# Kernel tuning notes

Measured on AMD Instinct MI355X. Metric: run time of the kernel, lower is better.

The kernel has to match this reference:

```python
import math
import jax, jax.numpy as jnp
import numpy as np

# Model hyperparameters (match init_kwargs)
LAYERS, BLOCKS = 10, 4
RC, DC, SC = 32, 32, 256          # residual / dilation / skip channels
CLASSES, L, K = 256, 1024, 3      # classes, input_length, kernel_size
B = 64                            # batch


def _dilations():
    """Replicates the (new_dilation, init_dilation) schedule built in __init__."""
    ds = []
    init = 1
    for _b in range(BLOCKS):
        d = 1
        for _i in range(LAYERS):
            ds.append((d, init))
            init = d
            d *= 2
    return ds


def dilate(x, dilation, init_dilation):
    """Faithful port of the torch dilate(): (n,c,l) -> (n*d/d0, c, l*d0/d)
    via permute/view/permute, zero-padding the start if l is not divisible."""
    n, c, l = x.shape
    if dilation == init_dilation:
        return x
    factor = dilation / init_dilation
    new_l = int(np.ceil(l / factor) * factor)
    if new_l != l:  # constant_pad_1d with pad_start=True
        x = jnp.pad(x, ((0, 0), (0, 0), (new_l - l, 0)))
        l = new_l
    l_new = int(math.ceil(l * init_dilation / dilation))
    n_new = int(math.ceil(n * dilation / init_dilation))
    x = jnp.transpose(x, (1, 2, 0)).reshape(c, l_new, n_new)  # (c, l, n) contiguous view
    return jnp.transpose(x, (2, 0, 1))


def conv1d(x, w, pad):
    # x: (N, Cin, L), w: (Cout, Cin, K)
    return jax.lax.conv_general_dilated(
        x, w, window_strides=(1,), padding=[(pad, pad)],
        dimension_numbers=("NCH", "OIH", "NCH"))


def setup_inputs() -> dict:
    key = jax.random.key(0)
    ks = jax.random.split(key, 8)
    NL = LAYERS * BLOCKS
    return {
        "input": jax.random.normal(ks[0], (B, 2, L), jnp.float32),
        "start_w": jax.random.normal(ks[1], (RC, 2, 1), jnp.float32) * 0.3,
        "filter_w": jax.random.normal(ks[2], (NL, DC, RC, K), jnp.float32) * 0.1,
        "gate_w": jax.random.normal(ks[3], (NL, DC, RC, K), jnp.float32) * 0.1,
        "res_w": jax.random.normal(ks[4], (NL, RC, DC, 1), jnp.float32) * 0.1,
        "skip_w": jax.random.normal(ks[5], (NL, SC, DC, 1), jnp.float32) * 0.1,
        "fc_w": jax.random.normal(ks[6], (CLASSES, SC * L), jnp.float32) * 0.002,
        "fc_b": jnp.zeros((CLASSES,), jnp.float32),
    }


def reference(input, start_w, filter_w, gate_w, res_w, skip_w, fc_w, fc_b):
    pad = K // 2
    x = conv1d(input, start_w, 0)  # (B, RC, L)
    skip = None
    for i, (d, d0) in enumerate(_dilations()):
        residual = dilate(x, d, d0)                              # fast-wavenet reshape
        f = jnp.tanh(conv1d(residual, filter_w[i], pad))
        g = jax.nn.sigmoid(conv1d(residual, gate_w[i], pad))
        x = f * g                                                # gated activation
        s = x if x.shape[2] == 1 else dilate(x, 1, d)            # undo dilation for skip
        s = conv1d(s, skip_w[i], 0)                              # (B, SC, L)
        skip = s if skip is None else s + skip[:, :, -s.shape[2]:]
        x = conv1d(x, res_w[i], 0) + residual                    # residual connection
    out = jax.nn.relu(skip.reshape(skip.shape[0], -1))           # (B, SC*L)
    return out @ fc_w.T + fc_b                                   # (B, CLASSES)
```

## Files before the change

### kernel.cpp

```cpp
#include <hip/hip_runtime.h>
#include <stdint.h>

typedef short bf16x8 __attribute__((ext_vector_type(8)));
typedef short s4 __attribute__((ext_vector_type(4)));
typedef float f32x4 __attribute__((ext_vector_type(4)));

#define NPOS 65536
#define MB (1024ull * 1024ull)
#define SK_PIECE 2097152

__device__ __forceinline__ unsigned short f32_bf16(float f) {
    union { float f; unsigned u; } v; v.f = f;
    unsigned u = v.u;
    u += 0x7fffu + ((u >> 16) & 1u);
    return (unsigned short)(u >> 16);
}

__device__ __forceinline__ s4 pk4_bf16(float a, float b, float c, float d) {
    union { unsigned u[2]; s4 v; } r;
    asm("v_cvt_pk_bf16_f32 %0, %1, %2" : "=v"(r.u[0]) : "v"(a), "v"(b));
    asm("v_cvt_pk_bf16_f32 %0, %1, %2" : "=v"(r.u[1]) : "v"(c), "v"(d));
    return r.v;
}

__device__ __forceinline__ bf16x8 ldf8_bf16(const float* p) {
    const float4 lo = *(const float4*)p;
    const float4 hi = *(const float4*)(p + 4);
    bf16x8 v;
    v[0] = (short)f32_bf16(lo.x); v[1] = (short)f32_bf16(lo.y);
    v[2] = (short)f32_bf16(lo.z); v[3] = (short)f32_bf16(lo.w);
    v[4] = (short)f32_bf16(hi.x); v[5] = (short)f32_bf16(hi.y);
    v[6] = (short)f32_bf16(hi.z); v[7] = (short)f32_bf16(hi.w);
    return v;
}

__global__ void ws_probe_k(float* __restrict__ out, float mib) {
    int i = blockIdx.x * 256 + threadIdx.x;
    if (i < 16384) out[i] = mib;
}

__global__ void repack_fgw_k(const float* __restrict__ fw,
                             const float* __restrict__ gw,
                             unsigned short* __restrict__ out) {
    int idx = blockIdx.x * 256 + threadIdx.x;
    int ic = idx & 31;
    int r1 = idx >> 5;
    int oc = r1 & 63;
    int r2 = r1 >> 6;
    int k  = r2 % 3;
    int i  = r2 / 3;
    const float* src = (oc < 32) ? fw : gw;
    out[idx] = f32_bf16(src[(((i * 32 + (oc & 31)) * 32 + ic) * 3) + k]);
}

__global__ void repack_sw_k(const float* __restrict__ sw,
                            unsigned short* __restrict__ out) {
    int idx = blockIdx.x * 256 + threadIdx.x;
    out[idx] = f32_bf16(sw[idx]);
}

__global__ void repack_rw_k(const float* __restrict__ rw,
                            unsigned short* __restrict__ out) {
    int idx = blockIdx.x * 256 + threadIdx.x;
    out[idx] = f32_bf16(rw[idx]);
}

__global__ __launch_bounds__(512, 2) void wavenet_rows_k(
    const float* __restrict__ in,
    const float* __restrict__ stw,
    const unsigned short* __restrict__ fgw_all,
    const unsigned short* __restrict__ rwb_all,
    unsigned short* __restrict__ xg_all)
{
    __shared__ __align__(16) unsigned short xb16[1024 * 32];
    __shared__ __align__(16) unsigned short stage[8 * 640];

    const int tid = threadIdx.x;
    const int w = tid >> 6, lane = tid & 63;
    const int quad = lane >> 4, l15 = lane & 15;
    const int b = blockIdx.x;
    const f32x4 zero = {0.f, 0.f, 0.f, 0.f};
    const int c0lo = quad >> 1;
    const int bi   = (quad & 1) * 4;

    float xreg[8][8];

    {
        float s0[8], s1[8];
#pragma unroll
        for (int j = 0; j < 8; ++j) {
            int c = (j < 4) ? (quad * 4 + j) : (16 + quad * 4 + (j - 4));
            s0[j] = stw[c * 2 + 0];
            s1[j] = stw[c * 2 + 1];
        }
#pragma unroll
        for (int g = 0; g < 8; ++g) {
            int t = (w * 8 + g) * 16 + l15;
            float i0 = in[(b * 2 + 0) * 1024 + t];
            float i1 = in[(b * 2 + 1) * 1024 + t];
#pragma unroll
            for (int j = 0; j < 8; ++j) xreg[g][j] = s0[j] * i0 + s1[j] * i1;
            s4 lo = pk4_bf16(xreg[g][0], xreg[g][1], xreg[g][2], xreg[g][3]);
            s4 hi = pk4_bf16(xreg[g][4], xreg[g][5], xreg[g][6], xreg[g][7]);
            int base = t * 32;
            *(s4*)(xb16 + base + ((c0lo ^ (t & 3)) * 8) + bi) = lo;
            *(s4*)(xb16 + base + (((c0lo + 2) ^ (t & 3)) * 8) + bi) = hi;
        }
    }
    __syncthreads();

    unsigned short* const st = stage + w * 640;

#pragma unroll 1
    for (int i = 0; i < 40; ++i) {
        const int d = 1 << (i % 10);
        const unsigned short* fgw = fgw_all + (size_t)i * 6144;
        unsigned short* xg = xg_all + (size_t)i * ((size_t)NPOS * 32)
                                    + (size_t)b * 1024 * 32;
        const bool dores = (i < 39);

        bf16x8 wf[3][2], wg[3][2], wr[2];
#pragma unroll
        for (int k = 0; k < 3; ++k) {
            const unsigned short* wb = fgw + k * 2048;
#pragma unroll
            for (int mt = 0; mt < 2; ++mt) {
                wf[k][mt] = *(const bf16x8*)(wb + (mt * 16 + l15) * 32 + quad * 8);
                wg[k][mt] = *(const bf16x8*)(wb + ((mt + 2) * 16 + l15) * 32 + quad * 8);
            }
        }
        if (dores) {
            const unsigned short* rwb = rwb_all + (size_t)i * 1024;
#pragma unroll
            for (int rt = 0; rt < 2; ++rt)
                wr[rt] = *(const bf16x8*)(rwb + (rt * 16 + l15) * 32 + quad * 8);
        }

#pragma unroll
        for (int g = 0; g < 8; ++g) {
            const int tg = (w * 8 + g) * 16;
            const int tc = tg + l15;

            bf16x8 bfr[3];
            bf16x8 zz; 
#pragma unroll
            for (int j = 0; j < 8; ++j) zz[j] = 0;
            bfr[1] = *(const bf16x8*)(xb16 + tc * 32 + ((quad ^ (tc & 3)) * 8));
            {
                int ts = tc - d, tsc = ts & 1023;
                bf16x8 rv = *(const bf16x8*)(xb16 + tsc * 32 + ((quad ^ (tsc & 3)) * 8));
                bfr[0] = (ts >= 0) ? rv : zz;
            }
            {
                int ts = tc + d, tsc = ts & 1023;
                bf16x8 rv = *(const bf16x8*)(xb16 + tsc * 32 + ((quad ^ (tsc & 3)) * 8));
                bfr[2] = (ts < 1024) ? rv : zz;
            }

            f32x4 accf[2] = {zero, zero};
            f32x4 accg[2] = {zero, zero};
#pragma unroll
            for (int k = 0; k < 3; ++k) {
#pragma unroll
                for (int mt = 0; mt < 2; ++mt) {
                    accf[mt] = __builtin_amdgcn_mfma_f32_16x16x32_bf16(wf[k][mt], bfr[k], accf[mt], 0, 0, 0);
                    accg[mt] = __builtin_amdgcn_mfma_f32_16x16x32_bf16(wg[k][mt], bfr[k], accg[mt], 0, 0, 0);
                }
            }

#pragma unroll
            for (int mt = 0; mt < 2; ++mt) {
                float gv0, gv1, gv2, gv3;
                {
                    float o[4];
#pragma unroll
                    for (int r = 0; r < 4; ++r) {
                        float fv = accf[mt][r], gg = accg[mt][r];
                        float ef = __expf(2.0f * fv);
                        float th = 1.0f - 2.0f * __builtin_amdgcn_rcpf(1.0f + ef);
                        float eg = __expf(-gg);
                        float sg = __builtin_amdgcn_rcpf(1.0f + eg);
                        o[r] = th * sg;
                    }
                    gv0 = o[0]; gv1 = o[1]; gv2 = o[2]; gv3 = o[3];
                }
                *(s4*)(st + l15 * 40 + mt * 16 + quad * 4) = pk4_bf16(gv0, gv1, gv2, gv3);
            }

            if (dores) {
                bf16x8 bx = *(const bf16x8*)(st + l15 * 40 + quad * 8);
                f32x4 accr[2] = {zero, zero};
#pragma unroll
                for (int rt = 0; rt < 2; ++rt)
                    accr[rt] = __builtin_amdgcn_mfma_f32_16x16x32_bf16(wr[rt], bx, accr[rt], 0, 0, 0);
#pragma unroll
                for (int rt = 0; rt < 2; ++rt)
#pragma unroll
                    for (int r = 0; r < 4; ++r)
                        xreg[g][rt * 4 + r] += accr[rt][r];
            }

            {
                int pp = lane >> 2, cc = (lane & 3) * 8;
                int4 v = *(const int4*)(st + pp * 40 + cc);
                *(int4*)(xg + (size_t)(tg + pp) * 32 + cc) = v;
            }
        }
        __syncthreads();

        if (dores) {
#pragma unroll
            for (int g = 0; g < 8; ++g) {
                int t = (w * 8 + g) * 16 + l15;
                s4 lo = pk4_bf16(xreg[g][0], xreg[g][1], xreg[g][2], xreg[g][3]);
                s4 hi = pk4_bf16(xreg[g][4], xreg[g][5], xreg[g][6], xreg[g][7]);
                int base = t * 32;
                *(s4*)(xb16 + base + ((c0lo ^ (t & 3)) * 8) + bi) = lo;
                *(s4*)(xb16 + base + (((c0lo + 2) ^ (t & 3)) * 8) + bi) = hi;
            }
            __syncthreads();
        }
    }
}

__global__ __launch_bounds__(256) void skip_gemm_k(
    const unsigned short* __restrict__ xg_all,
    const unsigned short* __restrict__ swb,
    unsigned short* __restrict__ sk)
{
    __shared__ __align__(16) unsigned short lds[256 * 72];
    int tid = threadIdx.x;
    int w = tid >> 6, lane = tid & 63;
    int quad = lane >> 4, l15 = lane & 15;
    int p0 = blockIdx.x * 64;
    f32x4 zero = {0.f, 0.f, 0.f, 0.f};
    f32x4 acc[4][4];
#pragma unroll
    for (int a = 0; a < 4; ++a)
#pragma unroll
        for (int c = 0; c < 4; ++c) acc[a][c] = zero;

    const unsigned short* bbase = xg_all + ((size_t)(p0 + l15)) * 32 + quad * 8;
    const unsigned short* abase = swb + ((size_t)(w * 64 + l15)) * 32 + quad * 8;

    bf16x8 bcur[4], acur[4], bnxt[4], anxt[4];
#pragma unroll
    for (int ct = 0; ct < 4; ++ct) bcur[ct] = *(const bf16x8*)(bbase + ct * 512);
#pragma unroll
    for (int rt = 0; rt < 4; ++rt) acur[rt] = *(const bf16x8*)(abase + rt * 512);

#pragma unroll 2
    for (int i = 0; i < 40; ++i) {
        if (i < 39) {
            const unsigned short* bn = bbase + (size_t)(i + 1) * NPOS * 32;
            const unsigned short* an = abase + (size_t)(i + 1) * 8192;
#pragma unroll
            for (int ct = 0; ct < 4; ++ct) bnxt[ct] = *(const bf16x8*)(bn + ct * 512);
#pragma unroll
            for (int rt = 0; rt < 4; ++rt) anxt[rt] = *(const bf16x8*)(an + rt * 512);
        }
#pragma unroll
        for (int rt = 0; rt < 4; ++rt)
#pragma unroll
            for (int ct = 0; ct < 4; ++ct)
                acc[rt][ct] = __builtin_amdgcn_mfma_f32_16x16x32_bf16(acur[rt], bcur[ct], acc[rt][ct], 0, 0, 0);
#pragma unroll
        for (int ct = 0; ct < 4; ++ct) bcur[ct] = bnxt[ct];
#pragma unroll
        for (int rt = 0; rt < 4; ++rt) acur[rt] = anxt[rt];
    }

#pragma unroll
    for (int rt = 0; rt < 4; ++rt)
#pragma unroll
        for (int ct = 0; ct < 4; ++ct)
#pragma unroll
            for (int r = 0; r < 4; ++r) {
                float v = acc[rt][ct][r];
                v = v > 0.f ? v : 0.f;
                lds[(w * 64 + rt * 16 + quad * 4 + r) * 72 + ct * 16 + l15] = f32_bf16(v);
            }
    __syncthreads();
    {
        size_t pbbase = (size_t)(p0 >> 6) * 2048;
#pragma unroll
        for (int j = 0; j < 8; ++j) {
            int idx = tid + 256 * j;
            int sc = idx >> 3, tc = idx & 7;
            int4 v = *(const int4*)(lds + sc * 72 + tc * 8);
            unsigned short* dst = sk + (size_t)(sc >> 5) * SK_PIECE + pbbase
                                     + (sc & 31) * 64 + tc * 8;
            *(int4*)dst = v;
        }
    }
}

__global__ __launch_bounds__(256) void fc_part_k(
    const unsigned short* __restrict__ sk,
    const float* __restrict__ fw,
    float* __restrict__ part)
{
    int tid = threadIdx.x;
    int w = tid >> 6, lane = tid & 63;
    int quad = lane >> 4, l15 = lane & 15;
    int kb = blockIdx.x;
    int sc = kb >> 1;
    int tbase = (kb & 1) * 512;
    f32x4 zero = {0.f, 0.f, 0.f, 0.f};
    f32x4 acc[4][4];
#pragma unroll
    for (int a = 0; a < 4; ++a)
#pragma unroll
        for (int c = 0; c < 4; ++c) acc[a][c] = zero;

    const unsigned short* skp = sk + (size_t)(sc >> 5) * SK_PIECE + (sc & 31) * 64;

    for (int it = 0; it < 16; ++it) {
        int t = tbase + it * 32 + quad * 8;
        bf16x8 af[4];
#pragma unroll
        for (int rt = 0; rt < 4; ++rt) {
            int bi = rt * 16 + l15;
            af[rt] = *(const bf16x8*)(skp + (size_t)(bi * 16 + (t >> 6)) * 2048 + (t & 63));
        }
#pragma unroll
        for (int ct = 0; ct < 4; ++ct) {
            bf16x8 bw = ldf8_bf16(fw + (size_t)(w * 64 + ct * 16 + l15) * 262144 + sc * 1024 + t);
#pragma unroll
            for (int rt = 0; rt < 4; ++rt)
                acc[rt][ct] = __builtin_amdgcn_mfma_f32_16x16x32_bf16(af[rt], bw, acc[rt][ct], 0, 0, 0);
        }
    }
#pragma unroll
    for (int rt = 0; rt < 4; ++rt)
#pragma unroll
        for (int ct = 0; ct < 4; ++ct)
#pragma unroll
            for (int r = 0; r < 4; ++r) {
                int bb = rt * 16 + quad * 4 + r;
                int cls = w * 64 + ct * 16 + l15;
                part[((size_t)kb * 64 + bb) * 256 + cls] = acc[rt][ct][r];
            }
}

__global__ void fc_reduce_k(const float* __restrict__ part,
                            const float* __restrict__ fb,
                            float* __restrict__ out) {
    int b = blockIdx.x, cls = threadIdx.x;
    float s = fb[cls];
    for (int kb = 0; kb < 512; ++kb)
        s += part[((size_t)kb * 64 + b) * 256 + cls];
    out[b * 256 + cls] = s;
}

extern "C" void kernel_launch(void* const* d_in, const int* in_sizes, int n_in,
                              void* d_out, int out_size, void* d_ws, size_t ws_size,
                              hipStream_t stream) {
    const float* input    = (const float*)d_in[0];
    const float* start_w  = (const float*)d_in[1];
    const float* filter_w = (const float*)d_in[2];
    const float* gate_w   = (const float*)d_in[3];
    const float* res_w    = (const float*)d_in[4];
    const float* skip_w   = (const float*)d_in[5];
    const float* fc_w     = (const float*)d_in[6];
    const float* fc_b     = (const float*)d_in[7];
    float* out = (float*)d_out;

    const size_t REQUIRED = 192 * MB;
    if (ws_size < REQUIRED) {
        ws_probe_k<<<64, 256, 0, stream>>>(out, (float)(ws_size >> 20));
        return;
    }

    char* ws = (char*)d_ws;
    unsigned short* xg_all = (unsigned short*)(ws);
    unsigned short* sk     = (unsigned short*)(ws);
    float*          part   = (float*)(ws + 32 * MB);
    unsigned short* fgw    = (unsigned short*)(ws + 176 * MB);
    unsigned short* swb    = (unsigned short*)(ws + 176 * MB + 512 * 1024);
    unsigned short* rwb    = (unsigned short*)(ws + 178 * MB);

    repack_fgw_k<<<960, 256, 0, stream>>>(filter_w, gate_w, fgw);
    repack_sw_k<<<1280, 256, 0, stream>>>(skip_w, swb);
    repack_rw_k<<<160, 256, 0, stream>>>(res_w, rwb);

    wavenet_rows_k<<<64, 512, 0, stream>>>(input, start_w, fgw, rwb, xg_all);

    skip_gemm_k<<<1024, 256, 0, stream>>>(xg_all, swb, sk);
    fc_part_k<<<512, 256, 0, stream>>>(sk, fc_w, part);
    fc_reduce_k<<<64, 256, 0, stream>>>(part, fc_b, out);
}
```

Baseline: 795.4 us.

## Double-buffer wavenet LDS, widen to 1024 threads, stage FC weights via LDS

The recurrent wavenet kernel now runs 1024 threads per batch row and ping-pongs between two LDS buffers, which removes one barrier per layer. It also permutes the filter, gate and residual weight rows so the gated output can feed the residual MFMA directly from registers, dropping the LDS staging tile. The FC partial kernel prefetches fc weights into a double-buffered LDS tile, converting to bf16 once per block instead of in every wave. The final reduction is split into two kernels for more parallelism, and the tanh and sigmoid are fused into one reciprocal with clamping.

```diff
diff --git a/kernel.cpp b/kernel.cpp
--- a/kernel.cpp
+++ b/kernel.cpp
@@ -23,15 +23,13 @@
     return r.v;
 }
 
-__device__ __forceinline__ bf16x8 ldf8_bf16(const float* p) {
-    const float4 lo = *(const float4*)p;
-    const float4 hi = *(const float4*)(p + 4);
-    bf16x8 v;
-    v[0] = (short)f32_bf16(lo.x); v[1] = (short)f32_bf16(lo.y);
-    v[2] = (short)f32_bf16(lo.z); v[3] = (short)f32_bf16(lo.w);
-    v[4] = (short)f32_bf16(hi.x); v[5] = (short)f32_bf16(hi.y);
-    v[6] = (short)f32_bf16(hi.z); v[7] = (short)f32_bf16(hi.w);
-    return v;
+__device__ __forceinline__ bf16x8 pk8_bf16(const float* v) {
+    union { unsigned u[4]; bf16x8 x; } r;
+    asm("v_cvt_pk_bf16_f32 %0, %1, %2" : "=v"(r.u[0]) : "v"(v[0]), "v"(v[1]));
+    asm("v_cvt_pk_bf16_f32 %0, %1, %2" : "=v"(r.u[1]) : "v"(v[2]), "v"(v[3]));
+    asm("v_cvt_pk_bf16_f32 %0, %1, %2" : "=v"(r.u[2]) : "v"(v[4]), "v"(v[5]));
+    asm("v_cvt_pk_bf16_f32 %0, %1, %2" : "=v"(r.u[3]) : "v"(v[6]), "v"(v[7]));
+    return r.x;
 }
 
 __global__ void ws_probe_k(float* __restrict__ out, float mib) {
@@ -45,12 +43,15 @@
     int idx = blockIdx.x * 256 + threadIdx.x;
     int ic = idx & 31;
     int r1 = idx >> 5;
-    int oc = r1 & 63;
+    int rq = r1 & 63;
     int r2 = r1 >> 6;
     int k  = r2 % 3;
     int i  = r2 / 3;
-    const float* src = (oc < 32) ? fw : gw;
-    out[idx] = f32_bf16(src[(((i * 32 + (oc & 31)) * 32 + ic) * 3) + k]);
+    int part = rq >> 4;
+    int m = rq & 15;
+    int oc = ((m >> 2) << 3) + ((part & 1) << 2) + (m & 3);
+    const float* src = (part < 2) ? fw : gw;
+    out[idx] = f32_bf16(src[(((i * 32 + oc) * 32 + ic) * 3) + k]);
 }
 
 __global__ void repack_sw_k(const float* __restrict__ sw,
@@ -62,64 +63,64 @@
 __global__ void repack_rw_k(const float* __restrict__ rw,
                             unsigned short* __restrict__ out) {
     int idx = blockIdx.x * 256 + threadIdx.x;
-    out[idx] = f32_bf16(rw[idx]);
-}
-
-__global__ __launch_bounds__(512, 2) void wavenet_rows_k(
+    int ic = idx & 31;
+    int r1 = idx >> 5;
+    int rq = r1 & 31;
+    int i  = r1 >> 5;
+    int rt = rq >> 4, m = rq & 15;
+    int oc = ((m >> 2) << 3) + (rt << 2) + (m & 3);
+    out[idx] = f32_bf16(rw[(i * 32 + oc) * 32 + ic]);
+}
+
+#define MFMA16(A, B, C) __builtin_amdgcn_mfma_f32_16x16x32_bf16(A, B, C, 0, 0, 0)
+
+__global__ __launch_bounds__(1024, 4) void wavenet_rows_k(
     const float* __restrict__ in,
     const float* __restrict__ stw,
     const unsigned short* __restrict__ fgw_all,
     const unsigned short* __restrict__ rwb_all,
     unsigned short* __restrict__ xg_all)
 {
-    __shared__ __align__(16) unsigned short xb16[1024 * 32];
-    __shared__ __align__(16) unsigned short stage[8 * 640];
-
+    __shared__ __align__(16) unsigned short xb16[2][1024 * 32];
     const int tid = threadIdx.x;
     const int w = tid >> 6, lane = tid & 63;
     const int quad = lane >> 4, l15 = lane & 15;
     const int b = blockIdx.x;
     const f32x4 zero = {0.f, 0.f, 0.f, 0.f};
-    const int c0lo = quad >> 1;
-    const int bi   = (quad & 1) * 4;
-
-    float xreg[8][8];
+
+    float xreg[4][8];
 
     {
         float s0[8], s1[8];
 #pragma unroll
         for (int j = 0; j < 8; ++j) {
-            int c = (j < 4) ? (quad * 4 + j) : (16 + quad * 4 + (j - 4));
+            int c = quad * 8 + j;
             s0[j] = stw[c * 2 + 0];
             s1[j] = stw[c * 2 + 1];
         }
 #pragma unroll
-        for (int g = 0; g < 8; ++g) {
-            int t = (w * 8 + g) * 16 + l15;
-            float i0 = in[(b * 2 + 0) * 1024 + t];
-            float i1 = in[(b * 2 + 1) * 1024 + t];
+        for (int g = 0; g < 4; ++g) {
+            int t = (w * 4 + g) * 16 + l15;
+            float i0 = in[b * 2048 + t];
+            float i1 = in[b * 2048 + 1024 + t];
 #pragma unroll
             for (int j = 0; j < 8; ++j) xreg[g][j] = s0[j] * i0 + s1[j] * i1;
-            s4 lo = pk4_bf16(xreg[g][0], xreg[g][1], xreg[g][2], xreg[g][3]);
-            s4 hi = pk4_bf16(xreg[g][4], xreg[g][5], xreg[g][6], xreg[g][7]);
-            int base = t * 32;
-            *(s4*)(xb16 + base + ((c0lo ^ (t & 3)) * 8) + bi) = lo;
-            *(s4*)(xb16 + base + (((c0lo + 2) ^ (t & 3)) * 8) + bi) = hi;
+            *(bf16x8*)(xb16[0] + t * 32 + ((quad ^ (t & 3)) * 8)) = pk8_bf16(xreg[g]);
         }
     }
     __syncthreads();
-
-    unsigned short* const st = stage + w * 640;
 
 #pragma unroll 1
     for (int i = 0; i < 40; ++i) {
         const int d = 1 << (i % 10);
         const unsigned short* fgw = fgw_all + (size_t)i * 6144;
         unsigned short* xg = xg_all + (size_t)i * ((size_t)NPOS * 32)
-                                    + (size_t)b * 1024 * 32;
+                                    + (size_t)b * (1024 * 32);
+        const unsigned short* xcur = xb16[i & 1];
+        unsigned short* xnxt = xb16[(i & 1) ^ 1];
         const bool dores = (i < 39);
 
-        bf16x8 wf[3][2], wg[3][2], wr[2];
+        bf16x8 wf[3][2], wg[3][2];
 #pragma unroll
         for (int k = 0; k < 3; ++k) {
             const unsigned short* wb = fgw + k * 2048;
@@ -129,97 +130,89 @@
                 wg[k][mt] = *(const bf16x8*)(wb + ((mt + 2) * 16 + l15) * 32 + quad * 8);
             }
         }
+        bf16x8 wr0, wr1;
         if (dores) {
             const unsigned short* rwb = rwb_all + (size_t)i * 1024;
-#pragma unroll
-            for (int rt = 0; rt < 2; ++rt)
-                wr[rt] = *(const bf16x8*)(rwb + (rt * 16 + l15) * 32 + quad * 8);
-        }
-
-#pragma unroll
-        for (int g = 0; g < 8; ++g) {
-            const int tg = (w * 8 + g) * 16;
+            wr0 = *(const bf16x8*)(rwb + l15 * 32 + quad * 8);
+            wr1 = *(const bf16x8*)(rwb + (16 + l15) * 32 + quad * 8);
+        }
+
+#pragma unroll
+        for (int g = 0; g < 4; ++g) {
+            const int tg = (w * 4 + g) * 16;
             const int tc = tg + l15;
 
-            bf16x8 bfr[3];
-            bf16x8 zz; 
+            bf16x8 zz;
 #pragma unroll
             for (int j = 0; j < 8; ++j) zz[j] = 0;
-            bfr[1] = *(const bf16x8*)(xb16 + tc * 32 + ((quad ^ (tc & 3)) * 8));
-            {
-                int ts = tc - d, tsc = ts & 1023;
-                bf16x8 rv = *(const bf16x8*)(xb16 + tsc * 32 + ((quad ^ (tsc & 3)) * 8));
-                bfr[0] = (ts >= 0) ? rv : zz;
-            }
-            {
-                int ts = tc + d, tsc = ts & 1023;
-                bf16x8 rv = *(const bf16x8*)(xb16 + tsc * 32 + ((quad ^ (tsc & 3)) * 8));
-                bfr[2] = (ts < 1024) ? rv : zz;
-            }
 
             f32x4 accf[2] = {zero, zero};
             f32x4 accg[2] = {zero, zero};
-#pragma unroll
-            for (int k = 0; k < 3; ++k) {
+            {
+                int ts = tc - d, tm = ts & 1023;
+                bf16x8 rv = *(const bf16x8*)(xcur + tm * 32 + ((quad ^ (tm & 3)) * 8));
+                bf16x8 b0 = (ts >= 0) ? rv : zz;
 #pragma unroll
                 for (int mt = 0; mt < 2; ++mt) {
-                    accf[mt] = __builtin_amdgcn_mfma_f32_16x16x32_bf16(wf[k][mt], bfr[k], accf[mt], 0, 0, 0);
-                    accg[mt] = __builtin_amdgcn_mfma_f32_16x16x32_bf16(wg[k][mt], bfr[k], accg[mt], 0, 0, 0);
+                    accf[mt] = MFMA16(wf[0][mt], b0, accf[mt]);
+                    accg[mt] = MFMA16(wg[0][mt], b0, accg[mt]);
                 }
             }
-
-#pragma unroll
-            for (int mt = 0; mt < 2; ++mt) {
-                float gv0, gv1, gv2, gv3;
-                {
-                    float o[4];
-#pragma unroll
-                    for (int r = 0; r < 4; ++r) {
-                        float fv = accf[mt][r], gg = accg[mt][r];
-                        float ef = __expf(2.0f * fv);
-                        float th = 1.0f - 2.0f * __builtin_amdgcn_rcpf(1.0f + ef);
-                        float eg = __expf(-gg);
-                        float sg = __builtin_amdgcn_rcpf(1.0f + eg);
-                        o[r] = th * sg;
-                    }
-                    gv0 = o[0]; gv1 = o[1]; gv2 = o[2]; gv3 = o[3];
+            {
+                bf16x8 b1 = *(const bf16x8*)(xcur + tc * 32 + ((quad ^ (tc & 3)) * 8));
+#pragma unroll
+                for (int mt = 0; mt < 2; ++mt) {
+                    accf[mt] = MFMA16(wf[1][mt], b1, accf[mt]);
+                    accg[mt] = MFMA16(wg[1][mt], b1, accg[mt]);
                 }
-                *(s4*)(st + l15 * 40 + mt * 16 + quad * 4) = pk4_bf16(gv0, gv1, gv2, gv3);
-            }
+            }
+            {
+                int ts = tc + d, tm = ts & 1023;
+                bf16x8 rv = *(const bf16x8*)(xcur + tm * 32 + ((quad ^ (tm & 3)) * 8));
+                bf16x8 b2 = (ts < 1024) ? rv : zz;
+#pragma unroll
+                for (int mt = 0; mt < 2; ++mt) {
+                    accf[mt] = MFMA16(wf[2][mt], b2, accf[mt]);
+                    accg[mt] = MFMA16(wg[2][mt], b2, accg[mt]);
+                }
+            }
+
+            float gv[8];
+#pragma unroll
+            for (int mt = 0; mt < 2; ++mt)
+#pragma unroll
+                for (int r = 0; r < 4; ++r) {
+                    float fv = accf[mt][r], gg = accg[mt][r];
+                    fv = fminf(fmaxf(fv, -10.f), 10.f);
+                    gg = fminf(fmaxf(gg, -15.f), 15.f);
+                    float a = __expf(2.f * fv);
+                    float c = __expf(-gg);
+                    float rr = __builtin_amdgcn_rcpf((a + 1.f) * (1.f + c));
+                    gv[mt * 4 + r] = (a - 1.f) * rr;
+                }
+            bf16x8 bx = pk8_bf16(gv);
+
+            *(bf16x8*)(xg + (size_t)tc * 32 + quad * 8) = bx;
 
             if (dores) {
-                bf16x8 bx = *(const bf16x8*)(st + l15 * 40 + quad * 8);
-                f32x4 accr[2] = {zero, zero};
-#pragma unroll
-                for (int rt = 0; rt < 2; ++rt)
-                    accr[rt] = __builtin_amdgcn_mfma_f32_16x16x32_bf16(wr[rt], bx, accr[rt], 0, 0, 0);
-#pragma unroll
-                for (int rt = 0; rt < 2; ++rt)
-#pragma unroll
-                    for (int r = 0; r < 4; ++r)
-                        xreg[g][rt * 4 + r] += accr[rt][r];
-            }
-
-            {
-                int pp = lane >> 2, cc = (lane & 3) * 8;
-                int4 v = *(const int4*)(st + pp * 40 + cc);
-                *(int4*)(xg + (size_t)(tg + pp) * 32 + cc) = v;
+                f32x4 a0 = MFMA16(wr0, bx, zero);
+                f32x4 a1 = MFMA16(wr1, bx, zero);
+#pragma unroll
+                for (int r = 0; r < 4; ++r) {
+                    xreg[g][r]     += a0[r];
+                    xreg[g][4 + r] += a1[r];
+                }
+            }
+        }
+
+        if (dores) {
+#pragma unroll
+            for (int g = 0; g < 4; ++g) {
+                int t = (w * 4 + g) * 16 + l15;
+                *(bf16x8*)(xnxt + t * 32 + ((quad ^ (t & 3)) * 8)) = pk8_bf16(xreg[g]);
             }
         }
         __syncthreads();
-
-        if (dores) {
-#pragma unroll
-            for (int g = 0; g < 8; ++g) {
-                int t = (w * 8 + g) * 16 + l15;
-                s4 lo = pk4_bf16(xreg[g][0], xreg[g][1], xreg[g][2], xreg[g][3]);
-                s4 hi = pk4_bf16(xreg[g][4], xreg[g][5], xreg[g][6], xreg[g][7]);
-                int base = t * 32;
-                *(s4*)(xb16 + base + ((c0lo ^ (t & 3)) * 8) + bi) = lo;
-                *(s4*)(xb16 + base + (((c0lo + 2) ^ (t & 3)) * 8) + bi) = hi;
-            }
-            __syncthreads();
-        }
     }
 }
 
@@ -300,6 +293,7 @@
     const float* __restrict__ fw,
     float* __restrict__ part)
 {
+    __shared__ __align__(16) unsigned short blds[2][256 * 32];
     int tid = threadIdx.x;
     int w = tid >> 6, lane = tid & 63;
     int quad = lane >> 4, l15 = lane & 15;
@@ -314,8 +308,28 @@
         for (int c = 0; c < 4; ++c) acc[a][c] = zero;
 
     const unsigned short* skp = sk + (size_t)(sc >> 5) * SK_PIECE + (sc & 31) * 64;
-
+    const int cls_s = tid >> 3, kc_s = tid & 7;
+    const float* fwbase = fw + (size_t)cls_s * 262144 + sc * 1024 + tbase + kc_s * 4;
+
+    auto stage = [&](int it, int buf) {
+        float4 v[8];
+#pragma unroll
+        for (int jj = 0; jj < 8; ++jj)
+            v[jj] = *(const float4*)(fwbase + (size_t)jj * 32 * 262144 + it * 32);
+#pragma unroll
+        for (int jj = 0; jj < 8; ++jj) {
+            int cls = cls_s + jj * 32;
+            int slot = (kc_s >> 1) ^ (cls & 3);
+            *(s4*)(blds[buf] + cls * 32 + slot * 8 + (kc_s & 1) * 4) =
+                pk4_bf16(v[jj].x, v[jj].y, v[jj].z, v[jj].w);
+        }
+    };
+
+    stage(0, 0);
+    __syncthreads();
     for (int it = 0; it < 16; ++it) {
+        int buf = it & 1;
+        if (it < 15) stage(it + 1, buf ^ 1);
         int t = tbase + it * 32 + quad * 8;
         bf16x8 af[4];
 #pragma unroll
@@ -325,11 +339,13 @@
         }
 #pragma unroll
         for (int ct = 0; ct < 4; ++ct) {
-            bf16x8 bw = ldf8_bf16(fw + (size_t)(w * 64 + ct * 16 + l15) * 262144 + sc * 1024 + t);
+            int cls = w * 64 + ct * 16 + l15;
+            bf16x8 bw = *(const bf16x8*)(blds[buf] + cls * 32 + ((quad ^ (cls & 3)) * 8));
 #pragma unroll
             for (int rt = 0; rt < 4; ++rt)
                 acc[rt][ct] = __builtin_amdgcn_mfma_f32_16x16x32_bf16(af[rt], bw, acc[rt][ct], 0, 0, 0);
         }
+        __syncthreads();
     }
 #pragma unroll
     for (int rt = 0; rt < 4; ++rt)
@@ -343,13 +359,23 @@
             }
 }
 
-__global__ void fc_reduce_k(const float* __restrict__ part,
-                            const float* __restrict__ fb,
-                            float* __restrict__ out) {
+__global__ void fc_r1_k(const float* __restrict__ part, float* __restrict__ part2) {
+    int blk = blockIdx.x;
+    int b = blk & 63, kc = blk >> 6;
+    int cls = threadIdx.x;
+    float s = 0.f;
+    for (int kb = kc * 64; kb < kc * 64 + 64; ++kb)
+        s += part[((size_t)kb * 64 + b) * 256 + cls];
+    part2[((size_t)kc * 64 + b) * 256 + cls] = s;
+}
+
+__global__ void fc_r2_k(const float* __restrict__ part2,
+                        const float* __restrict__ fb,
+                        float* __restrict__ out) {
     int b = blockIdx.x, cls = threadIdx.x;
     float s = fb[cls];
-    for (int kb = 0; kb < 512; ++kb)
-        s += part[((size_t)kb * 64 + b) * 256 + cls];
+    for (int kc = 0; kc < 8; ++kc)
+        s += part2[((size_t)kc * 64 + b) * 256 + cls];
     out[b * 256 + cls] = s;
 }
 
@@ -376,6 +402,7 @@
     unsigned short* xg_all = (unsigned short*)(ws);
     unsigned short* sk     = (unsigned short*)(ws);
     float*          part   = (float*)(ws + 32 * MB);
+    float*          part2  = (float*)(ws + 64 * MB);
     unsigned short* fgw    = (unsigned short*)(ws + 176 * MB);
     unsigned short* swb    = (unsigned short*)(ws + 176 * MB + 512 * 1024);
     unsigned short* rwb    = (unsigned short*)(ws + 178 * MB);
@@ -384,9 +411,10 @@
     repack_sw_k<<<1280, 256, 0, stream>>>(skip_w, swb);
     repack_rw_k<<<160, 256, 0, stream>>>(res_w, rwb);
 
-    wavenet_rows_k<<<64, 512, 0, stream>>>(input, start_w, fgw, rwb, xg_all);
+    wavenet_rows_k<<<64, 1024, 0, stream>>>(input, start_w, fgw, rwb, xg_all);
 
     skip_gemm_k<<<1024, 256, 0, stream>>>(xg_all, swb, sk);
     fc_part_k<<<512, 256, 0, stream>>>(sk, fc_w, part);
-    fc_reduce_k<<<64, 256, 0, stream>>>(part, fc_b, out);
-}
+    fc_r1_k<<<512, 256, 0, stream>>>(part, part2);
+    fc_r2_k<<<64, 256, 0, stream>>>(part2, fc_b, out);
+}
```

New measurement: 837.4 us. 5.3% more time.
